# Kernel tuning notes

Hardware: AMD Instinct MI355X
Metric: run time of the kernel (lower is better)

## Reference

```python
import jax, jax.numpy as jnp
import numpy as np

B, T, IN_DIM, EMBED, OUT_DIM, WS = 32, 512, 2048, 512, 29, 64


def setup_inputs() -> dict:
    key = jax.random.key(0)
    ks = jax.random.split(key, 8)
    x = jax.random.normal(ks[0], (B, T, IN_DIM), dtype=jnp.float32)
    # pack_padded_sequence contract: lengths sorted descending, max length == T
    lens = jnp.sort(jax.random.randint(ks[1], (B,), T // 2, T + 1))[::-1]
    sample_lengths = lens.at[0].set(T).astype(jnp.int64)
    s_in = 1.0 / np.sqrt(IN_DIM)
    s_q = 1.0 / np.sqrt(OUT_DIM)
    s_o = 1.0 / np.sqrt(EMBED)
    return {
        "x": x,
        "sample_lengths": sample_lengths,
        "W_in": jax.random.normal(ks[2], (IN_DIM, EMBED), jnp.float32) * s_in,
        "b_in": jnp.zeros((EMBED,), jnp.float32),
        "W_q": jax.random.normal(ks[3], (OUT_DIM, EMBED), jnp.float32) * s_q,
        "b_q": jnp.zeros((EMBED,), jnp.float32),
        "W_out": jax.random.normal(ks[4], (EMBED, OUT_DIM), jnp.float32) * s_o,
        "b_out": jnp.zeros((OUT_DIM,), jnp.float32),
        "window_size": WS,
    }


def reference(x, sample_lengths, W_in, b_in, W_q, b_q, W_out, b_out, window_size):
    # x: [B, T, input_dim] padded (pad_packed_sequence equivalent)
    Bb, Tt, _ = x.shape
    D = W_in.shape[1]
    h = x @ W_in + b_in                       # input_proj, [B, T, D]
    lens = sample_lengths
    j = jnp.arange(Tt)
    scale = 1.0 / jnp.sqrt(jnp.asarray(D, h.dtype))
    neg = jnp.finfo(h.dtype).min
    # generate_query0 with init_strategy='fix': ones, last channel = 9
    q0 = jnp.ones((Bb, 1, W_q.shape[0]), h.dtype).at[:, :, -1].set(9.0)

    def step(query, t):
        q = query @ W_q + b_q                 # query_proj, [B, 1, D]
        scores = jnp.einsum('bod,btd->bot', q, h) * scale  # [B, 1, T]
        # local window around query index t, clipped to each sequence length
        valid = (j >= t - window_size) & (j <= t + window_size) & (j[None, :] < lens[:, None])
        w = jax.nn.softmax(jnp.where(valid[:, None, :], scores, neg), axis=-1)
        alive = (t < lens).astype(h.dtype)[:, None, None]  # finished seqs -> zeros (blank_out/blank_wgts)
        out = jnp.einsum('bot,btd->bod', w, h) * alive      # [B, 1, D]
        new_query = out @ W_out + b_out        # output_proj, [B, 1, 29]
        return new_query, (new_query[:, 0, :], (w * alive)[:, 0, :])

    _, (outs, wgts) = jax.lax.scan(step, q0, jnp.arange(Tt))
    outputs = jnp.transpose(outs, (1, 0, 2))   # [B, T, 29]
    weights = jnp.transpose(wgts, (1, 0, 2))   # [B, T, T]
    return outputs, weights
```

## Files before the change

kernel.cpp:

```cpp
#include <hip/hip_runtime.h>
#include <math.h>

#define BB 32
#define TT 512
#define IND 2048
#define DD 512
#define OD 29
#define WCOLS 64
#define PTS 516

typedef float v2f __attribute__((ext_vector_type(2)));

__device__ __forceinline__ v2f pk_fma(v2f a, v2f b, v2f c) {
  v2f d;
  asm("v_pk_fma_f32 %0, %1, %2, %3" : "=v"(d) : "v"(a), "v"(b), "v"(c));
  return d;
}

template<int CTRL, int RM>
__device__ __forceinline__ float updpp(float idv, float x) {
  return __int_as_float(__builtin_amdgcn_update_dpp(
      __float_as_int(idv), __float_as_int(x), CTRL, RM, 0xf, false));
}

__device__ __forceinline__ float red_max64(float x) {
  const float ID = -3.0e38f;
  x = fmaxf(x, updpp<0xB1, 0xf>(ID, x));
  x = fmaxf(x, updpp<0x4E, 0xf>(ID, x));
  x = fmaxf(x, updpp<0x124, 0xf>(ID, x));
  x = fmaxf(x, updpp<0x128, 0xf>(ID, x));
  x = fmaxf(x, updpp<0x142, 0xa>(ID, x));
  x = fmaxf(x, updpp<0x143, 0xc>(ID, x));
  return __int_as_float(__builtin_amdgcn_readlane(__float_as_int(x), 63));
}

__device__ __forceinline__ float red_sum64(float x) {
  x += updpp<0xB1, 0xf>(0.f, x);
  x += updpp<0x4E, 0xf>(0.f, x);
  x += updpp<0x124, 0xf>(0.f, x);
  x += updpp<0x128, 0xf>(0.f, x);
  x += updpp<0x142, 0xa>(0.f, x);
  x += updpp<0x143, 0xc>(0.f, x);
  return __int_as_float(__builtin_amdgcn_readlane(__float_as_int(x), 63));
}

__global__ void k_zero(float* __restrict__ p, int n) {
  int n4 = n >> 2;
  int i = blockIdx.x * blockDim.x + threadIdx.x;
  int stride = gridDim.x * blockDim.x;
  float4 z = make_float4(0.f, 0.f, 0.f, 0.f);
  for (int j = i; j < n4; j += stride) ((float4*)p)[j] = z;
  int base = (n4 << 2) + i;
  if (base < n) p[base] = 0.f;
}

__global__ __launch_bounds__(64) void k_transform(
    const float* __restrict__ W_in, const float* __restrict__ b_in,
    const float* __restrict__ W_q,  const float* __restrict__ b_q,
    const float* __restrict__ W_out, float* __restrict__ Wt) {
  int i = blockIdx.x;
  int c = threadIdx.x;
  const float* row = (i < IND) ? (W_in + (size_t)i * DD) : b_in;
  const float* m;
  int strd;
  bool valid = true, dscale = false;
  if (c < OD)                { m = W_q + (size_t)c * DD; strd = 1; dscale = true; }
  else if (c == OD)          { m = b_q;                  strd = 1; dscale = true; }
  else if (c >= 32 && c < 32 + OD) { m = W_out + (c - 32); strd = OD; }
  else                       { m = b_q; strd = 0; valid = false; }
  float a0 = 0.f, a1 = 0.f, a2 = 0.f, a3 = 0.f;
  for (int d = 0; d < DD; d += 4) {
    a0 += row[d + 0] * m[(size_t)(d + 0) * strd];
    a1 += row[d + 1] * m[(size_t)(d + 1) * strd];
    a2 += row[d + 2] * m[(size_t)(d + 2) * strd];
    a3 += row[d + 3] * m[(size_t)(d + 3) * strd];
  }
  float acc = (a0 + a1) + (a2 + a3);
  if (dscale) acc *= (1.0f / sqrtf((float)DD));
  if (!valid) acc = 0.f;
  Wt[(size_t)i * WCOLS + c] = acc;
}

__global__ __launch_bounds__(256) void k_gemm(
    const float* __restrict__ x, const float* __restrict__ Wt,
    float* __restrict__ GPC) {
  __shared__ float xt[128][65];
  int tid = threadIdx.x;
  int r = tid & 63;
  int cg16 = __builtin_amdgcn_readfirstlane((tid >> 6) << 4);
  int m0 = blockIdx.x << 6;
  int lr = tid >> 2, lc = tid & 3;
  const float* xl = x + (size_t)(m0 + lr) * IND;
  float4 a0 = make_float4(0,0,0,0), a1 = a0, a2 = a0, a3 = a0;
  for (int kk = 0; kk < IND; kk += 128) {
    __syncthreads();
    #pragma unroll
    for (int j = 0; j < 8; ++j) {
      int k = (lc + 4 * j) << 2;
      float4 v = *(const float4*)(xl + kk + k);
      xt[k + 0][lr] = v.x; xt[k + 1][lr] = v.y;
      xt[k + 2][lr] = v.z; xt[k + 3][lr] = v.w;
    }
    __syncthreads();
    const float* wb = Wt + (size_t)kk * WCOLS + cg16;
    #pragma unroll 4
    for (int k = 0; k < 128; ++k) {
      float xv = xt[k][r];
      const float* wk = wb + (size_t)k * WCOLS;
      float4 w0 = *(const float4*)(wk + 0);
      float4 w1 = *(const float4*)(wk + 4);
      float4 w2 = *(const float4*)(wk + 8);
      float4 w3 = *(const float4*)(wk + 12);
      a0.x += xv * w0.x; a0.y += xv * w0.y; a0.z += xv * w0.z; a0.w += xv * w0.w;
      a1.x += xv * w1.x; a1.y += xv * w1.y; a1.z += xv * w1.z; a1.w += xv * w1.w;
      a2.x += xv * w2.x; a2.y += xv * w2.y; a2.z += xv * w2.z; a2.w += xv * w2.w;
      a3.x += xv * w3.x; a3.y += xv * w3.y; a3.z += xv * w3.z; a3.w += xv * w3.w;
    }
  }
  const float* br = Wt + (size_t)IND * WCOLS + cg16;
  float4 b0 = *(const float4*)(br + 0), b1 = *(const float4*)(br + 4);
  float4 b2 = *(const float4*)(br + 8), b3 = *(const float4*)(br + 12);
  a0.x += b0.x; a0.y += b0.y; a0.z += b0.z; a0.w += b0.w;
  a1.x += b1.x; a1.y += b1.y; a1.z += b1.z; a1.w += b1.w;
  a2.x += b2.x; a2.y += b2.y; a2.z += b2.z; a2.w += b2.w;
  a3.x += b3.x; a3.y += b3.y; a3.z += b3.z; a3.w += b3.w;
  float* o = GPC + (size_t)(m0 + r) * WCOLS + cg16;
  *(float4*)(o + 0) = a0; *(float4*)(o + 4)  = a1;
  *(float4*)(o + 8) = a2; *(float4*)(o + 12) = a3;
}

__device__ __forceinline__ void ld_g(v2f* g, const float* gb, int j) {
  const float4* s = (const float4*)(gb + (size_t)j * WCOLS);
  #pragma unroll
  for (int u = 0; u < 8; ++u) {
    float4 v = s[u];
    g[2*u+0] = (v2f){v.x, v.y};
    g[2*u+1] = (v2f){v.z, v.w};
  }
}

__device__ __forceinline__ float score_pk(const v2f* g, const v2f* qp) {
  v2f a0 = pk_fma(qp[0], g[0], (v2f){0.f, 0.f});
  v2f a1 = pk_fma(qp[1], g[1], (v2f){0.f, 0.f});
  v2f a2 = pk_fma(qp[2], g[2], (v2f){0.f, 0.f});
  #pragma unroll
  for (int i = 3; i < 15; i += 3) {
    a0 = pk_fma(qp[i+0], g[i+0], a0);
    a1 = pk_fma(qp[i+1], g[i+1], a1);
    a2 = pk_fma(qp[i+2], g[i+2], a2);
  }
  v2f s = a0 + a1;
  s = s + a2;
  return s.x + s.y;
}

__global__ __launch_bounds__(64, 1) void k_scan(
    const float* __restrict__ GPC, const int* __restrict__ lens_raw,
    const float* __restrict__ b_out, const int* __restrict__ wsp,
    float* __restrict__ outputs, float* __restrict__ weights) {
  __shared__ __align__(16) float Pt[OD * PTS];
  __shared__ __align__(16) float w_lds[640];

  int b = blockIdx.x;
  int l = threadIdx.x;
  int len;
  {
    int probe = lens_raw[1];
    len = (probe == 0) ? lens_raw[2 * b] : lens_raw[b];
  }
  if (len > TT) len = TT;
  if (len < 0) len = 0;
  int ws = wsp[0];

  const float* gb = GPC + (size_t)b * TT * WCOLS;
  for (int j0 = 0; j0 < TT; j0 += 64) {
    int j = j0 + l;
    const float* src = gb + (size_t)j * WCOLS + 32;
    #pragma unroll
    for (int u = 0; u < 8; ++u) {
      float4 v = *(const float4*)(src + 4 * u);
      int kb = 4 * u;
      if (kb + 0 < OD) Pt[(kb+0)*PTS + j] = v.x;
      if (kb + 1 < OD) Pt[(kb+1)*PTS + j] = v.y;
      if (kb + 2 < OD) Pt[(kb+2)*PTS + j] = v.z;
      if (kb + 3 < OD) Pt[(kb+3)*PTS + j] = v.w;
    }
  }
  for (int j = l; j < 640; j += 64) w_lds[j] = 0.f;
  __syncthreads();

  int k = l & 31, h = l >> 5;
  float boutk = (k < OD) ? b_out[k] : 0.f;

  float* outb = outputs + (size_t)b * TT * OD;
  float* wb   = weights + (size_t)b * TT * TT;

  v2f qp[15];
  #pragma unroll
  for (int i = 0; i < 14; ++i) qp[i] = (v2f){1.f, 1.f};
  qp[14] = (v2f){9.f, 1.f};

  v2f g0[16], g1[16], g2[16];
  int j0r = l, j1r = 64 + l, j2r = 128 + l;
  ld_g(g0, gb, j0r); ld_g(g1, gb, j1r); ld_g(g2, gb, j2r);

  int jlo = 0;
  int jhi = (ws < len - 1) ? ws : (len - 1);

  float m_run = -3.0e38f;
  int t = 0;
  for (; t < len; ++t) {
    float s0 = score_pk(g0, qp);
    float s1 = score_pk(g1, qp);
    float s2 = score_pk(g2, qp);
    bool v0 = (j0r >= jlo) & (j0r <= jhi);
    bool v1 = (j1r >= jlo) & (j1r <= jhi);
    bool v2 = (j2r >= jlo) & (j2r <= jhi);
    const float NEG = -3.0e38f;
    float mx0 = fmaxf(fmaxf(v0 ? s0 : NEG, v1 ? s1 : NEG), v2 ? s2 : NEG);
    float mx = m_run;
    float e0 = v0 ? __expf(s0 - mx) : 0.f;
    float e1 = v1 ? __expf(s1 - mx) : 0.f;
    float e2 = v2 ? __expf(s2 - mx) : 0.f;
    if (!(__all(mx0 <= m_run + 8.0f) && __any(mx0 >= m_run - 20.0f))) {
      mx = red_max64(mx0);
      m_run = mx;
      e0 = v0 ? __expf(s0 - mx) : 0.f;
      e1 = v1 ? __expf(s1 - mx) : 0.f;
      e2 = v2 ? __expf(s2 - mx) : 0.f;
    }
    if (l == 0 && jlo > 0) w_lds[jlo - 1] = 0.f;
    if (v0) w_lds[j0r] = e0;
    if (v1) w_lds[j1r] = e1;
    if (v2) w_lds[j2r] = e2;
    float sm = red_sum64(e0 + e1 + e2);
    float invS = __builtin_amdgcn_rcpf(sm);
    v2f p01 = (v2f){0.f, 0.f}, p23 = (v2f){0.f, 0.f};
    int qlo = jlo >> 2;
    if (k < OD) {
      const float* pr = Pt + k * PTS + ((qlo + h) << 2);
      const float* wr = w_lds + ((qlo + h) << 2);
      #pragma unroll
      for (int i = 0; i < 17; ++i) {
        float4 wv = *(const float4*)(wr + (i << 3));
        float4 pv = *(const float4*)(pr + (i << 3));
        p01 = pk_fma((v2f){wv.x, wv.y}, (v2f){pv.x, pv.y}, p01);
        p23 = pk_fma((v2f){wv.z, wv.w}, (v2f){pv.z, pv.w}, p23);
      }
    }
    float tot = (p01.x + p01.y) + (p23.x + p23.y);
    tot += __shfl_xor(tot, 32);
    float nq = tot * invS + boutk;
    if (h == 0 && k < OD) outb[(size_t)t * OD + k] = nq;
    float* wrow = wb + (size_t)t * TT;
    if (v0) wrow[j0r] = e0 * invS;
    if (v1) wrow[j1r] = e1 * invS;
    if (v2) wrow[j2r] = e2 * invS;
    int jnew = t + 2 + ws;
    if (jnew >= 192 && jnew < TT) {
      int sl = (jnew >> 6) % 3;
      int ln = jnew & 63;
      if (sl == 0)      { if (l == ln) { ld_g(g0, gb, jnew); j0r = jnew; } }
      else if (sl == 1) { if (l == ln) { ld_g(g1, gb, jnew); j1r = jnew; } }
      else              { if (l == ln) { ld_g(g2, gb, jnew); j2r = jnew; } }
    }
    #pragma unroll
    for (int kk = 0; kk < 14; ++kk) {
      float lo = __int_as_float(__builtin_amdgcn_readlane(__float_as_int(nq), 2*kk));
      float hi = __int_as_float(__builtin_amdgcn_readlane(__float_as_int(nq), 2*kk+1));
      qp[kk] = (v2f){lo, hi};
    }
    qp[14] = (v2f){__int_as_float(__builtin_amdgcn_readlane(__float_as_int(nq), 28)), 1.0f};
    jlo = (t + 1) - ws; if (jlo < 0) jlo = 0;
    jhi = (t + 1) + ws; if (jhi > len - 1) jhi = len - 1;
  }
  for (; t < TT; ++t)
    if (l < OD) outb[(size_t)t * OD + l] = boutk;
}

extern "C" void kernel_launch(void* const* d_in, const int* in_sizes, int n_in,
                              void* d_out, int out_size, void* d_ws, size_t ws_size,
                              hipStream_t stream) {
  const float* x     = (const float*)d_in[0];
  const int*   lens  = (const int*)d_in[1];
  const float* W_in  = (const float*)d_in[2];
  const float* b_in  = (const float*)d_in[3];
  const float* W_q   = (const float*)d_in[4];
  const float* b_q   = (const float*)d_in[5];
  const float* W_out = (const float*)d_in[6];
  const float* b_out = (const float*)d_in[7];
  const int*   wsp   = (const int*)d_in[8];
  float* out = (float*)d_out;

  float* Wt  = (float*)d_ws;
  float* GPC = Wt + (size_t)(IND + 1) * WCOLS;

  k_zero<<<1024, 256, 0, stream>>>(out, out_size);
  k_transform<<<IND + 1, 64, 0, stream>>>(W_in, b_in, W_q, b_q, W_out, Wt);
  k_gemm<<<(BB * TT) / 64, 256, 0, stream>>>(x, Wt, GPC);

  float* outputs = out;
  float* weights = out + (size_t)BB * TT * OD;
  k_scan<<<BB, 64, 0, stream>>>(GPC, lens, b_out, wsp, outputs, weights);
}
```

Baseline: 883.9 us.

## Pack eight sequences per scan block and stream transposed projections from global

Result: slower. 2.102 ms (+137.8%).

```diff
diff --git a/kernel.cpp b/kernel.cpp
--- a/kernel.cpp
+++ b/kernel.cpp
@@ -7,7 +7,8 @@
 #define DD 512
 #define OD 29
 #define WCOLS 64
-#define PTS 516
+#define GC 32
+#define PTL 640
 
 typedef float v2f __attribute__((ext_vector_type(2)));
 
@@ -83,7 +84,7 @@
 
 __global__ __launch_bounds__(256) void k_gemm(
     const float* __restrict__ x, const float* __restrict__ Wt,
-    float* __restrict__ GPC) {
+    float* __restrict__ GPC, float* __restrict__ Ptg) {
   __shared__ float xt[128][65];
   int tid = threadIdx.x;
   int r = tid & 63;
@@ -124,13 +125,25 @@
   a1.x += b1.x; a1.y += b1.y; a1.z += b1.z; a1.w += b1.w;
   a2.x += b2.x; a2.y += b2.y; a2.z += b2.z; a2.w += b2.w;
   a3.x += b3.x; a3.y += b3.y; a3.z += b3.z; a3.w += b3.w;
-  float* o = GPC + (size_t)(m0 + r) * WCOLS + cg16;
-  *(float4*)(o + 0) = a0; *(float4*)(o + 4)  = a1;
-  *(float4*)(o + 8) = a2; *(float4*)(o + 12) = a3;
+  if (cg16 < 32) {
+    float* o = GPC + (size_t)(m0 + r) * GC + cg16;
+    *(float4*)(o + 0) = a0; *(float4*)(o + 4) = a1;
+    *(float4*)(o + 8) = a2; *(float4*)(o + 12) = a3;
+  } else {
+    int bb = m0 >> 9;
+    int jj = (m0 & 511) + r;
+    int c0 = cg16 - 32;
+    float va[16] = {a0.x,a0.y,a0.z,a0.w, a1.x,a1.y,a1.z,a1.w,
+                    a2.x,a2.y,a2.z,a2.w, a3.x,a3.y,a3.z,a3.w};
+    #pragma unroll
+    for (int cc = 0; cc < 16; ++cc)
+      if (c0 + cc < OD)
+        Ptg[((size_t)bb * OD + c0 + cc) * PTL + jj] = va[cc];
+  }
 }
 
 __device__ __forceinline__ void ld_g(v2f* g, const float* gb, int j) {
-  const float4* s = (const float4*)(gb + (size_t)j * WCOLS);
+  const float4* s = (const float4*)(gb + (size_t)j * GC);
   #pragma unroll
   for (int u = 0; u < 8; ++u) {
     float4 v = s[u];
@@ -154,15 +167,18 @@
   return s.x + s.y;
 }
 
-__global__ __launch_bounds__(64, 1) void k_scan(
-    const float* __restrict__ GPC, const int* __restrict__ lens_raw,
+__global__ __launch_bounds__(512, 2) void k_scan(
+    const float* __restrict__ GPC, const float* __restrict__ Ptg,
+    const int* __restrict__ lens_raw,
     const float* __restrict__ b_out, const int* __restrict__ wsp,
     float* __restrict__ outputs, float* __restrict__ weights) {
-  __shared__ __align__(16) float Pt[OD * PTS];
-  __shared__ __align__(16) float w_lds[640];
-
-  int b = blockIdx.x;
-  int l = threadIdx.x;
+  __shared__ __align__(16) float w_all[8][PTL];
+
+  int wvu = __builtin_amdgcn_readfirstlane((int)(threadIdx.x >> 6));
+  int l   = threadIdx.x & 63;
+  int b   = blockIdx.x * 8 + wvu;
+  float* w_lds = w_all[wvu];
+
   int len;
   {
     int probe = lens_raw[1];
@@ -172,24 +188,12 @@
   if (len < 0) len = 0;
   int ws = wsp[0];
 
-  const float* gb = GPC + (size_t)b * TT * WCOLS;
-  for (int j0 = 0; j0 < TT; j0 += 64) {
-    int j = j0 + l;
-    const float* src = gb + (size_t)j * WCOLS + 32;
-    #pragma unroll
-    for (int u = 0; u < 8; ++u) {
-      float4 v = *(const float4*)(src + 4 * u);
-      int kb = 4 * u;
-      if (kb + 0 < OD) Pt[(kb+0)*PTS + j] = v.x;
-      if (kb + 1 < OD) Pt[(kb+1)*PTS + j] = v.y;
-      if (kb + 2 < OD) Pt[(kb+2)*PTS + j] = v.z;
-      if (kb + 3 < OD) Pt[(kb+3)*PTS + j] = v.w;
-    }
-  }
-  for (int j = l; j < 640; j += 64) w_lds[j] = 0.f;
-  __syncthreads();
+  const float* gb = GPC + (size_t)b * TT * GC;
+  for (int j = l; j < PTL; j += 64) w_lds[j] = 0.f;
 
   int k = l & 31, h = l >> 5;
+  int kc = (k < OD) ? k : (OD - 1);
+  const float* pvb = Ptg + ((size_t)b * OD + kc) * PTL;
   float boutk = (k < OD) ? b_out[k] : 0.f;
 
   float* outb = outputs + (size_t)b * TT * OD;
@@ -210,9 +214,16 @@
   float m_run = -3.0e38f;
   int t = 0;
   for (; t < len; ++t) {
+    int base = (jlo >> 2) << 2;
+    const float* pr = pvb + base + (h << 2);
+    float4 rpA[9], rpB[8];
+    #pragma unroll
+    for (int i = 0; i < 9; ++i) rpA[i] = *(const float4*)(pr + (i << 3));
     float s0 = score_pk(g0, qp);
     float s1 = score_pk(g1, qp);
     float s2 = score_pk(g2, qp);
+    #pragma unroll
+    for (int i = 0; i < 8; ++i) rpB[i] = *(const float4*)(pr + ((i + 9) << 3));
     bool v0 = (j0r >= jlo) & (j0r <= jhi);
     bool v1 = (j1r >= jlo) & (j1r <= jhi);
     bool v2 = (j2r >= jlo) & (j2r <= jhi);
@@ -235,27 +246,40 @@
     if (v2) w_lds[j2r] = e2;
     float sm = red_sum64(e0 + e1 + e2);
     float invS = __builtin_amdgcn_rcpf(sm);
-    v2f p01 = (v2f){0.f, 0.f}, p23 = (v2f){0.f, 0.f};
-    int qlo = jlo >> 2;
-    if (k < OD) {
-      const float* pr = Pt + k * PTS + ((qlo + h) << 2);
-      const float* wr = w_lds + ((qlo + h) << 2);
-      #pragma unroll
-      for (int i = 0; i < 17; ++i) {
-        float4 wv = *(const float4*)(wr + (i << 3));
-        float4 pv = *(const float4*)(pr + (i << 3));
-        p01 = pk_fma((v2f){wv.x, wv.y}, (v2f){pv.x, pv.y}, p01);
-        p23 = pk_fma((v2f){wv.z, wv.w}, (v2f){pv.z, pv.w}, p23);
-      }
-    }
-    float tot = (p01.x + p01.y) + (p23.x + p23.y);
-    tot += __shfl_xor(tot, 32);
-    float nq = tot * invS + boutk;
-    if (h == 0 && k < OD) outb[(size_t)t * OD + k] = nq;
     float* wrow = wb + (size_t)t * TT;
     if (v0) wrow[j0r] = e0 * invS;
     if (v1) wrow[j1r] = e1 * invS;
     if (v2) wrow[j2r] = e2 * invS;
+    v2f p01 = (v2f){0.f, 0.f}, p23 = (v2f){0.f, 0.f};
+    {
+      const float* wr = w_lds + base + (h << 2);
+      #pragma unroll
+      for (int i = 0; i < 9; ++i) {
+        float4 wv = *(const float4*)(wr + (i << 3));
+        p01 = pk_fma((v2f){wv.x, wv.y}, (v2f){rpA[i].x, rpA[i].y}, p01);
+        p23 = pk_fma((v2f){wv.z, wv.w}, (v2f){rpA[i].z, rpA[i].w}, p23);
+      }
+      #pragma unroll
+      for (int i = 0; i < 8; ++i) {
+        float4 wv = *(const float4*)(wr + ((i + 9) << 3));
+        p01 = pk_fma((v2f){wv.x, wv.y}, (v2f){rpB[i].x, rpB[i].y}, p01);
+        p23 = pk_fma((v2f){wv.z, wv.w}, (v2f){rpB[i].z, rpB[i].w}, p23);
+      }
+    }
+    float tot = (p01.x + p01.y) + (p23.x + p23.y);
+    float tc = tot;
+    asm("v_permlane32_swap_b32 %0, %1" : "+v"(tot), "+v"(tc));
+    float comb = ((l < 32) ? tot : tc);
+    comb = comb + ((l < 32) ? tc : tot);
+    float nq = comb * invS + boutk;
+    if (h == 0 && k < OD) outb[(size_t)t * OD + k] = nq;
+    #pragma unroll
+    for (int kk = 0; kk < 14; ++kk) {
+      float lo = __int_as_float(__builtin_amdgcn_readlane(__float_as_int(nq), 2*kk));
+      float hi = __int_as_float(__builtin_amdgcn_readlane(__float_as_int(nq), 2*kk+1));
+      qp[kk] = (v2f){lo, hi};
+    }
+    qp[14] = (v2f){__int_as_float(__builtin_amdgcn_readlane(__float_as_int(nq), 28)), 1.0f};
     int jnew = t + 2 + ws;
     if (jnew >= 192 && jnew < TT) {
       int sl = (jnew >> 6) % 3;
@@ -264,13 +288,6 @@
       else if (sl == 1) { if (l == ln) { ld_g(g1, gb, jnew); j1r = jnew; } }
       else              { if (l == ln) { ld_g(g2, gb, jnew); j2r = jnew; } }
     }
-    #pragma unroll
-    for (int kk = 0; kk < 14; ++kk) {
-      float lo = __int_as_float(__builtin_amdgcn_readlane(__float_as_int(nq), 2*kk));
-      float hi = __int_as_float(__builtin_amdgcn_readlane(__float_as_int(nq), 2*kk+1));
-      qp[kk] = (v2f){lo, hi};
-    }
-    qp[14] = (v2f){__int_as_float(__builtin_amdgcn_readlane(__float_as_int(nq), 28)), 1.0f};
     jlo = (t + 1) - ws; if (jlo < 0) jlo = 0;
     jhi = (t + 1) + ws; if (jhi > len - 1) jhi = len - 1;
   }
@@ -294,12 +311,13 @@
 
   float* Wt  = (float*)d_ws;
   float* GPC = Wt + (size_t)(IND + 1) * WCOLS;
+  float* Ptg = GPC + (size_t)BB * TT * GC;
 
   k_zero<<<1024, 256, 0, stream>>>(out, out_size);
   k_transform<<<IND + 1, 64, 0, stream>>>(W_in, b_in, W_q, b_q, W_out, Wt);
-  k_gemm<<<(BB * TT) / 64, 256, 0, stream>>>(x, Wt, GPC);
+  k_gemm<<<(BB * TT) / 64, 256, 0, stream>>>(x, Wt, GPC, Ptg);
 
   float* outputs = out;
   float* weights = out + (size_t)BB * TT * OD;
-  k_scan<<<BB, 64, 0, stream>>>(GPC, lens, b_out, wsp, outputs, weights);
-}
+  k_scan<<<BB / 8, 512, 0, stream>>>(GPC, Ptg, lens, b_out, wsp, outputs, weights);
+}
```
